# Kernel optimization log

Hardware: AMD Instinct MI355X
Metric: run time of the kernel (lower is better)

The kernel has to match this reference:

```python
import jax, jax.numpy as jnp
import numpy as np

N_HEADS = 32
N_KV = 8
N_REP = N_HEADS // N_KV  # 4
HEAD_DIM = 128
DIM = 4096


def _rope(x, cos, sin, start_pos):
    # x: (B, H, T, hd); cos/sin: (max_seq, hd//2)
    T = x.shape[2]
    c = jax.lax.dynamic_slice_in_dim(cos, start_pos, T, axis=0)[None, None]  # (1,1,T,hd/2)
    s = jax.lax.dynamic_slice_in_dim(sin, start_pos, T, axis=0)[None, None]
    x1, x2 = x[..., : HEAD_DIM // 2], x[..., HEAD_DIM // 2:]
    return jnp.concatenate([x1 * c - x2 * s, x2 * c + x1 * s], axis=-1)


def setup_inputs() -> dict:
    key = jax.random.key(0)
    ks = jax.random.split(key, 7)
    B, T = 1, 2048
    sc = 0.02
    return {
        "x": jax.random.normal(ks[0], (B, T, DIM), jnp.float32),
        "cos": jax.random.normal(ks[1], (T, HEAD_DIM // 2), jnp.float32),
        "sin": jax.random.normal(ks[2], (T, HEAD_DIM // 2), jnp.float32),
        "wq": jax.random.normal(ks[3], (N_HEADS * HEAD_DIM, DIM), jnp.float32) * sc,
        "wk": jax.random.normal(ks[4], (N_KV * HEAD_DIM, DIM), jnp.float32) * sc,
        "wv": jax.random.normal(ks[5], (N_KV * HEAD_DIM, DIM), jnp.float32) * sc,
        "wo": jax.random.normal(ks[6], (DIM, DIM), jnp.float32) * sc,
        "start_pos": 0,
    }


def reference(x, cos, sin, wq, wk, wv, wo, start_pos):
    B, T, _ = x.shape
    # Projections (nn.Linear: y = x @ W^T)
    q = (x @ wq.T).reshape(B, T, N_HEADS, HEAD_DIM).transpose(0, 2, 1, 3)  # (B,Hq,T,hd)
    k = (x @ wk.T).reshape(B, T, N_KV, HEAD_DIM).transpose(0, 2, 1, 3)    # (B,Hk,T,hd)
    v = (x @ wv.T).reshape(B, T, N_KV, HEAD_DIM).transpose(0, 2, 1, 3)
    q = _rope(q, cos, sin, start_pos)
    k = _rope(k, cos, sin, start_pos)
    # GQA: group query heads per kv head instead of materializing repeat_kv
    qg = q.reshape(B, N_KV, N_REP, T, HEAD_DIM)
    scale = 1.0 / jnp.sqrt(jnp.float32(HEAD_DIM))
    scores = jnp.einsum('bgrqd,bgkd->bgrqk', qg, k) * scale  # (B,Hk,rep,T,T)
    causal = jnp.tril(jnp.ones((T, T), dtype=bool))
    scores = jnp.where(causal, scores, jnp.finfo(scores.dtype).min)
    attn = jax.nn.softmax(scores, axis=-1)
    yg = jnp.einsum('bgrqk,bgkd->bgrqd', attn, v)  # (B,Hk,rep,T,hd)
    y = yg.reshape(B, N_HEADS, T, HEAD_DIM).transpose(0, 2, 1, 3).reshape(B, T, DIM)
    return y @ wo.T
```

## Files before the change

kernel.cpp:

```cpp
#include <hip/hip_runtime.h>
#include <hip/hip_bf16.h>
#include <stdint.h>

using bf16 = __hip_bfloat16;
using bf16x8 = __attribute__((ext_vector_type(8))) short;
using f32x4  = __attribute__((ext_vector_type(4))) float;

#define AS1 __attribute__((address_space(1)))
#define AS3 __attribute__((address_space(3)))

__device__ __forceinline__ void async_ld16(const void* g, void* l) {
    __builtin_amdgcn_global_load_lds((const AS1 void*)g, (AS3 void*)l, 16, 0, 0);
}

__device__ __forceinline__ f32x4 mfma_bf16(bf16x8 a, bf16x8 b, f32x4 c) {
    return __builtin_amdgcn_mfma_f32_16x16x32_bf16(a, b, c, 0, 0, 0);
}

__device__ __forceinline__ float sexp(float x) {
    return __expf(fmaxf(x, -80.0f));
}

template<int N> __device__ __forceinline__ float dpp_max16(float x) {
    int xi = __builtin_bit_cast(int, x);
    int yi = __builtin_amdgcn_update_dpp(xi, xi, 0x110 | N, 0xf, 0xf, false);
    return fmaxf(x, __builtin_bit_cast(float, yi));
}
template<int N> __device__ __forceinline__ float dpp_add16(float x) {
    int xi = __builtin_bit_cast(int, x);
    int yi = __builtin_amdgcn_update_dpp(0, xi, 0x110 | N, 0xf, 0xf, true);
    return x + __builtin_bit_cast(float, yi);
}
__device__ __forceinline__ float bcast15(float x) {
    return __builtin_bit_cast(float,
        __builtin_amdgcn_ds_swizzle(__builtin_bit_cast(int, x), 0x01F0));
}
__device__ __forceinline__ float redmax16(float x) {
    x = dpp_max16<1>(x); x = dpp_max16<2>(x);
    x = dpp_max16<4>(x); x = dpp_max16<8>(x);
    return bcast15(x);
}
__device__ __forceinline__ float redsum16(float x) {
    x = dpp_add16<1>(x); x = dpp_add16<2>(x);
    x = dpp_add16<4>(x); x = dpp_add16<8>(x);
    return bcast15(x);
}

__device__ __forceinline__ void cvt8(const float* p, bf16* d) {
    float4 lo = *(const float4*)p;
    float4 hi = *(const float4*)(p + 4);
    bf16 t8[8] = {__float2bfloat16(lo.x), __float2bfloat16(lo.y),
                  __float2bfloat16(lo.z), __float2bfloat16(lo.w),
                  __float2bfloat16(hi.x), __float2bfloat16(hi.y),
                  __float2bfloat16(hi.z), __float2bfloat16(hi.w)};
    *(bf16x8*)d = *(const bf16x8*)t8;
}

__global__ __launch_bounds__(256) void cvt4_k(const float* __restrict__ x,  bf16* __restrict__ xb,
                                              const float* __restrict__ wq, bf16* __restrict__ wqb,
                                              const float* __restrict__ wk, bf16* __restrict__ wkb,
                                              const float* __restrict__ wv, bf16* __restrict__ wvb) {
    int stride = gridDim.x * blockDim.x;
    for (int u = blockIdx.x * blockDim.x + threadIdx.x; u < 4194304; u += stride) {
        const float* s; bf16* d; size_t off;
        if (u < 1048576)      { s = x;  d = xb;  off = (size_t)u * 8; }
        else if (u < 3145728) { s = wq; d = wqb; off = (size_t)(u - 1048576) * 8; }
        else if (u < 3670016) { s = wk; d = wkb; off = (size_t)(u - 3145728) * 8; }
        else                  { s = wv; d = wvb; off = (size_t)(u - 3670016) * 8; }
        cvt8(s + off, d + off);
    }
}

__global__ __launch_bounds__(256) void cvt_f32_bf16(const float* __restrict__ src,
                                                    bf16* __restrict__ dst, int n8) {
    int stride = gridDim.x * blockDim.x;
    for (int u = blockIdx.x * blockDim.x + threadIdx.x; u < n8; u += stride)
        cvt8(src + (size_t)u * 8, dst + (size_t)u * 8);
}

template<bool SRCF32>
__device__ __forceinline__ void stage_tile(const void* __restrict__ src,
                                           bf16* __restrict__ s,
                                           int row0, int K, int k0, int tid) {
    if constexpr (SRCF32) {
        const float* g = (const float*)src;
        #pragma unroll
        for (int i = 0; i < 2; ++i) {
            int u = tid + 256 * i;
            int row = u >> 2, c8 = (u & 3) * 8;
            cvt8(g + (size_t)(row0 + row) * K + k0 + c8, &s[row * 32 + c8]);
        }
    } else {
        const bf16* g = (const bf16*)src;
        const int wave = tid >> 6, lane = tid & 63;
        const int c0 = wave * 64 + lane;
        const int r0 = c0 >> 2, cb0 = (c0 & 3) * 16;
        const int c1 = 256 + c0;
        const int r1 = c1 >> 2, cb1 = (c1 & 3) * 16;
        async_ld16((const char*)(g + (size_t)(row0 + r0) * K + k0) + cb0,
                   (char*)s + wave * 1024);
        async_ld16((const char*)(g + (size_t)(row0 + r1) * K + k0) + cb1,
                   (char*)s + 4096 + wave * 1024);
    }
}

template<bool AF32, bool BF32, int MODE>
__global__ __launch_bounds__(256) void gemm_bt(const void* __restrict__ A,
                                               const void* __restrict__ B,
                                               void* __restrict__ C,
                                               bf16* __restrict__ Qp,
                                               bf16* __restrict__ Kp,
                                               bf16* __restrict__ Vp,
                                               int M, int N, int K) {
    __shared__ bf16 sA[128 * 32];
    __shared__ bf16 sB[128 * 32];
    const int tid  = threadIdx.x;
    const int lane = tid & 63;
    const int wave = tid >> 6;
    const int m0 = blockIdx.y * 128;
    const int n0 = blockIdx.x * 128;
    const int mrow = (wave >> 1) * 64;
    const int ncol = (wave & 1) * 64;

    f32x4 acc[4][4] = {};

    for (int k0 = 0; k0 < K; k0 += 32) {
        __syncthreads();
        stage_tile<AF32>(A, sA, m0, K, k0, tid);
        stage_tile<BF32>(B, sB, n0, K, k0, tid);
        __syncthreads();

        bf16x8 af[4], bfr[4];
        #pragma unroll
        for (int i = 0; i < 4; ++i)
            af[i] = *(const bf16x8*)&sA[(mrow + i * 16 + (lane & 15)) * 32 + (lane >> 4) * 8];
        #pragma unroll
        for (int j = 0; j < 4; ++j)
            bfr[j] = *(const bf16x8*)&sB[(ncol + j * 16 + (lane & 15)) * 32 + (lane >> 4) * 8];
        #pragma unroll
        for (int i = 0; i < 4; ++i)
            #pragma unroll
            for (int j = 0; j < 4; ++j)
                acc[i][j] = mfma_bf16(af[i], bfr[j], acc[i][j]);
    }

    #pragma unroll
    for (int i = 0; i < 4; ++i)
        #pragma unroll
        for (int j = 0; j < 4; ++j)
            #pragma unroll
            for (int r = 0; r < 4; ++r) {
                int row = m0 + mrow + i * 16 + (lane >> 4) * 4 + r;
                int col = n0 + ncol + j * 16 + (lane & 15);
                float fv = acc[i][j][r];
                if constexpr (MODE == 0) {
                    ((bf16*)C)[(size_t)row * N + col] = __float2bfloat16(fv);
                } else if constexpr (MODE == 1) {
                    ((bf16*)C)[(size_t)col * M + row] = __float2bfloat16(fv);
                } else if constexpr (MODE == 2) {
                    bf16 v = __float2bfloat16(fv);
                    if (col < 4096)      Qp[(size_t)row * 4096 + col] = v;
                    else if (col < 5120) Kp[(size_t)row * 1024 + (col - 4096)] = v;
                    else                 Vp[(size_t)(col - 5120) * 2048 + row] = v;
                } else {
                    ((float*)C)[(size_t)row * N + col] = fv;
                }
            }
}

#define VMW(N) asm volatile("s_waitcnt vmcnt(" #N ")" ::: "memory")

#define PH(SA, SB, MH, NH, STG, WT) do {                                          \
    bf16x8 aF[2][2], bF[2][2];                                                    \
    _Pragma("unroll") for (int i2 = 0; i2 < 2; ++i2)                              \
      _Pragma("unroll") for (int kh = 0; kh < 2; ++kh)                            \
        aF[i2][kh] = *(const bf16x8*)((SA) + offA[(MH)*2 + i2][kh]);              \
    _Pragma("unroll") for (int j2 = 0; j2 < 2; ++j2)                              \
      _Pragma("unroll") for (int kh = 0; kh < 2; ++kh)                            \
        bF[j2][kh] = *(const bf16x8*)((SB) + offB[(NH)*2 + j2][kh]);              \
    STG;                                                                          \
    __builtin_amdgcn_s_barrier();                                                 \
    asm volatile("s_waitcnt lgkmcnt(0)" ::: "memory");                            \
    __builtin_amdgcn_sched_barrier(0);                                            \
    __builtin_amdgcn_s_setprio(1);                                                \
    _Pragma("unroll") for (int i2 = 0; i2 < 2; ++i2)                              \
      _Pragma("unroll") for (int j2 = 0; j2 < 2; ++j2)                            \
        _Pragma("unroll") for (int kh = 0; kh < 2; ++kh)                          \
          acc[(MH)*2 + i2][(NH)*2 + j2] =                                         \
              mfma_bf16(aF[i2][kh], bF[j2][kh], acc[(MH)*2 + i2][(NH)*2 + j2]);   \
    __builtin_amdgcn_s_setprio(0);                                                \
    __builtin_amdgcn_sched_barrier(0);                                            \
    WT;                                                                           \
    __builtin_amdgcn_s_barrier();                                                 \
  } while (0)

#define TILE(SA, SB, SA2, SB2, T2, DOST, WT) do {                                 \
    PH(SA, SB, 0, 0, if (DOST) stgA01(SA2, T2), );                                \
    PH(SA, SB, 0, 1, if (DOST) stgA23(SA2, T2), );                                \
    PH(SA, SB, 1, 0, if (DOST) stgB0(SB2, T2), );                                 \
    PH(SA, SB, 1, 1, if (DOST) stgB1(SB2, T2), WT);                               \
  } while (0)

template<int MODE>
__global__ __launch_bounds__(512, 1) void gemm_8p(const bf16* __restrict__ A,
                                                  const bf16* __restrict__ B,
                                                  void* __restrict__ C,
                                                  bf16* __restrict__ Qp,
                                                  bf16* __restrict__ Kp,
                                                  bf16* __restrict__ Vp,
                                                  int M, int N, int K) {
    __shared__ __align__(16) bf16 sA0[16384], sA1[16384], sA2[16384];
    __shared__ __align__(16) bf16 sB0[8192],  sB1[8192],  sB2[8192];

    const int tid  = threadIdx.x;
    const int lane = tid & 63;
    const int wave = tid >> 6;
    const int wr   = wave >> 1;
    const int wc   = wave & 1;
    const int m0 = blockIdx.y * 256;
    const int n0 = blockIdx.x * 128;
    const int NT = K >> 6;

    int offA[4][2], offB[4][2];
    {
        const int l15 = lane & 15, l4 = lane >> 4;
        #pragma unroll
        for (int i = 0; i < 4; ++i) {
            const int ra = wr * 64 + i * 16 + l15;
            const int rb = wc * 64 + i * 16 + l15;
            #pragma unroll
            for (int kh = 0; kh < 2; ++kh) {
                offA[i][kh] = ra * 64 + (((kh * 4 + l4) ^ (ra & 7)) * 8);
                offB[i][kh] = rb * 64 + (((kh * 4 + l4) ^ (rb & 7)) * 8);
            }
        }
    }

    const int rloc = tid >> 3;
    const int qsw  = (tid & 7) ^ (rloc & 7);
    const bf16* gA0 = A + (size_t)(m0 +   0 + rloc) * K + qsw * 8;
    const bf16* gA1 = A + (size_t)(m0 +  64 + rloc) * K + qsw * 8;
    const bf16* gA2 = A + (size_t)(m0 + 128 + rloc) * K + qsw * 8;
    const bf16* gA3 = A + (size_t)(m0 + 192 + rloc) * K + qsw * 8;
    const bf16* gB0 = B + (size_t)(n0 +   0 + rloc) * K + qsw * 8;
    const bf16* gB1 = B + (size_t)(n0 +  64 + rloc) * K + qsw * 8;
    const int w512 = wave * 512;

    auto stgA01 = [&](bf16* dst, int kt) __attribute__((always_inline)) {
        async_ld16(gA0 + kt * 64, dst + w512);
        async_ld16(gA1 + kt * 64, dst + 4096 + w512);
    };
    auto stgA23 = [&](bf16* dst, int kt) __attribute__((always_inline)) {
        async_ld16(gA2 + kt * 64, dst + 8192 + w512);
        async_ld16(gA3 + kt * 64, dst + 12288 + w512);
    };
    auto stgB0 = [&](bf16* dst, int kt) __attribute__((always_inline)) {
        async_ld16(gB0 + kt * 64, dst + w512);
    };
    auto stgB1 = [&](bf16* dst, int kt) __attribute__((always_inline)) {
        async_ld16(gB1 + kt * 64, dst + 4096 + w512);
    };

    f32x4 acc[4][4] = {};

    stgA01(sA0, 0); stgA23(sA0, 0); stgB0(sB0, 0); stgB1(sB0, 0);
    stgA01(sA1, 1); stgA23(sA1, 1); stgB0(sB1, 1); stgB1(sB1, 1);
    VMW(6);
    __builtin_amdgcn_s_barrier();
    asm volatile("" ::: "memory");
    __builtin_amdgcn_sched_barrier(0);

    int t = 0;
    for (; t < NT - 6; t += 3) {
        TILE(sA0, sB0, sA2, sB2, t + 2, true, VMW(6));
        TILE(sA1, sB1, sA0, sB0, t + 3, true, VMW(6));
        TILE(sA2, sB2, sA1, sB1, t + 4, true, VMW(6));
    }
    TILE(sA0, sB0, sA2, sB2, NT - 2, true,  VMW(6));
    TILE(sA1, sB1, sA0, sB0, NT - 1, true,  VMW(6));
    TILE(sA2, sB2, sA0, sB0, 0,      false, VMW(0));
    TILE(sA0, sB0, sA1, sB1, 0,      false, );
    asm volatile("s_waitcnt vmcnt(0)" ::: "memory");

    #pragma unroll
    for (int i = 0; i < 4; ++i)
        #pragma unroll
        for (int j = 0; j < 4; ++j)
            #pragma unroll
            for (int r = 0; r < 4; ++r) {
                int row = m0 + wr * 64 + i * 16 + (lane >> 4) * 4 + r;
                int col = n0 + wc * 64 + j * 16 + (lane & 15);
                float fv = acc[i][j][r];
                if constexpr (MODE == 2) {
                    bf16 v = __float2bfloat16(fv);
                    if (col < 4096)      Qp[(size_t)row * 4096 + col] = v;
                    else if (col < 5120) Kp[(size_t)row * 1024 + (col - 4096)] = v;
                    else                 Vp[(size_t)(col - 5120) * 2048 + row] = v;
                } else {
                    ((float*)C)[(size_t)row * N + col] = fv;
                }
            }
}

__global__ __launch_bounds__(256) void rope_all(bf16* __restrict__ Q,
                                                bf16* __restrict__ K,
                                                const float* __restrict__ cosp,
                                                const float* __restrict__ sinp,
                                                const int* __restrict__ spp) {
    int idx = blockIdx.x * blockDim.x + threadIdx.x;
    int d = idx & 63;
    int h = (idx >> 6) % 40;
    int t = idx / (64 * 40);
    int sp = *spp;
    float c = cosp[(size_t)(t + sp) * 64 + d];
    float s = sinp[(size_t)(t + sp) * 64 + d];
    bf16* row = (h < 32) ? (Q + (size_t)t * 4096 + h * 128)
                         : (K + (size_t)t * 1024 + (h - 32) * 128);
    float x1 = __bfloat162float(row[d]);
    float x2 = __bfloat162float(row[64 + d]);
    row[d]      = __float2bfloat16(x1 * c - x2 * s);
    row[64 + d] = __float2bfloat16(x2 * c + x1 * s);
}

#define NEG_SENT (-1.0e9f)
__global__ __launch_bounds__(256) void attn_k(const bf16* __restrict__ Q,
                                              const bf16* __restrict__ K,
                                              const bf16* __restrict__ VT,
                                              bf16* __restrict__ Y) {
    constexpr int SKS = 136;
    constexpr int SVS = 72;
    __shared__ bf16 sK[64 * SKS];
    __shared__ bf16 sVT[128 * SVS];

    const int tid  = threadIdx.x;
    const int lane = tid & 63;
    const int wave = tid >> 6;
    const int qtile = 31 - (blockIdx.x >> 5);
    const int head  = blockIdx.x & 31;
    const int g     = head >> 2;
    const int qrow0 = qtile * 64 + wave * 16;
    bf16* sPw = sK + wave * 1152;

    bf16x8 qf[4];
    {
        const bf16* qbase = Q + (size_t)(qrow0 + (lane & 15)) * 4096 + head * 128;
        #pragma unroll
        for (int kk = 0; kk < 4; ++kk)
            qf[kk] = *(const bf16x8*)(qbase + kk * 32 + (lane >> 4) * 8);
    }

    float m_i[4], l_i[4];
    #pragma unroll
    for (int r = 0; r < 4; ++r) { m_i[r] = NEG_SENT; l_i[r] = 0.f; }
    f32x4 o[8] = {};
    const float scale = 0.08838834764831845f;

    for (int kt = 0; kt <= qtile; ++kt) {
        const int kt0 = kt * 64;
        __syncthreads();
        #pragma unroll
        for (int i = 0; i < 4; ++i) {
            int c = i * 256 + tid;
            {
                int row = c >> 4, ch = c & 15;
                *(uint4*)&sK[row * SKS + ch * 8] =
                    *(const uint4*)(K + (size_t)(kt0 + row) * 1024 + g * 128 + ch * 8);
            }
            {
                int row = c >> 3, ch = c & 7;
                *(uint4*)&sVT[row * SVS + ch * 8] =
                    *(const uint4*)(VT + (size_t)(g * 128 + row) * 2048 + kt0 + ch * 8);
            }
        }
        __syncthreads();

        f32x4 s[4];
        #pragma unroll
        for (int j = 0; j < 4; ++j) {
            f32x4 a = {};
            #pragma unroll
            for (int kk = 0; kk < 4; ++kk) {
                bf16x8 kfrag = *(const bf16x8*)&sK[(j * 16 + (lane & 15)) * SKS +
                                                   kk * 32 + (lane >> 4) * 8];
                a = mfma_bf16(qf[kk], kfrag, a);
            }
            s[j] = a;
        }

        #pragma unroll
        for (int j = 0; j < 4; ++j) {
            int tk = kt0 + j * 16 + (lane & 15);
            #pragma unroll
            for (int r = 0; r < 4; ++r) {
                int tq = qrow0 + (lane >> 4) * 4 + r;
                float v = s[j][r] * scale;
                s[j][r] = (tk > tq) ? NEG_SENT : v;
            }
        }

        #pragma unroll
        for (int r = 0; r < 4; ++r) {
            float mx = fmaxf(fmaxf(s[0][r], s[1][r]), fmaxf(s[2][r], s[3][r]));
            mx = redmax16(mx);
            float mn = fmaxf(m_i[r], mx);
            float alpha = sexp(m_i[r] - mn);
            m_i[r] = mn;
            float rs = 0.f;
            #pragma unroll
            for (int j = 0; j < 4; ++j) {
                float pv = sexp(s[j][r] - mn);
                s[j][r] = pv;
                rs += pv;
            }
            l_i[r] = l_i[r] * alpha + rs;
            #pragma unroll
            for (int j2 = 0; j2 < 8; ++j2) o[j2][r] *= alpha;
        }

        __syncthreads();

        #pragma unroll
        for (int j = 0; j < 4; ++j)
            #pragma unroll
            for (int r = 0; r < 4; ++r)
                sPw[((lane >> 4) * 4 + r) * SVS + j * 16 + (lane & 15)] =
                    __float2bfloat16(s[j][r]);
        __asm__ volatile("s_waitcnt lgkmcnt(0)" ::: "memory");

        #pragma unroll
        for (int kk2 = 0; kk2 < 2; ++kk2) {
            bf16x8 pf = *(const bf16x8*)&sPw[(lane & 15) * SVS + kk2 * 32 + (lane >> 4) * 8];
            #pragma unroll
            for (int j2 = 0; j2 < 8; ++j2) {
                bf16x8 vf = *(const bf16x8*)&sVT[(j2 * 16 + (lane & 15)) * SVS +
                                                 kk2 * 32 + (lane >> 4) * 8];
                o[j2] = mfma_bf16(pf, vf, o[j2]);
            }
        }
    }

    #pragma unroll
    for (int r = 0; r < 4; ++r) l_i[r] = redsum16(l_i[r]);
    #pragma unroll
    for (int j2 = 0; j2 < 8; ++j2)
        #pragma unroll
        for (int r = 0; r < 4; ++r) {
            int t   = qrow0 + (lane >> 4) * 4 + r;
            int col = head * 128 + j2 * 16 + (lane & 15);
            Y[(size_t)t * 4096 + col] = __float2bfloat16(o[j2][r] / l_i[r]);
        }
}

extern "C" void kernel_launch(void* const* d_in, const int* in_sizes, int n_in,
                              void* d_out, int out_size, void* d_ws, size_t ws_size,
                              hipStream_t stream) {
    const float* x    = (const float*)d_in[0];
    const float* cosp = (const float*)d_in[1];
    const float* sinp = (const float*)d_in[2];
    const float* wq   = (const float*)d_in[3];
    const float* wk   = (const float*)d_in[4];
    const float* wv   = (const float*)d_in[5];
    const float* wo   = (const float*)d_in[6];
    const int*   sp   = (const int*)d_in[7];
    float* out = (float*)d_out;

    char* ws = (char*)d_ws;
    bf16* Qb = (bf16*)d_out;

    const size_t NEED = 92274688;
    if (ws_size >= NEED) {
        bf16* xb   = (bf16*)(ws);
        bf16* wqkv = (bf16*)(ws + (16u << 20));
        bf16* wob  = wqkv;
        bf16* Kb   = (bf16*)(ws + (64u << 20));
        bf16* VT   = (bf16*)(ws + (68u << 20));
        bf16* Yb   = (bf16*)(ws + (72u << 20));

        cvt4_k<<<dim3(4096), 256, 0, stream>>>(x, xb, wq, wqkv,
                                               wk, wqkv + 16777216, wv, wqkv + 20971520);

        gemm_8p<2><<<dim3(48, 8), 512, 0, stream>>>(
            xb, wqkv, nullptr, Qb, Kb, VT, 2048, 6144, 4096);

        cvt_f32_bf16<<<dim3(4096), 256, 0, stream>>>(wo, wob, 2097152);

        rope_all<<<dim3(2048 * 40 * 64 / 256), 256, 0, stream>>>(Qb, Kb, cosp, sinp, sp);

        attn_k<<<dim3(1024), 256, 0, stream>>>(Qb, Kb, VT, Yb);

        gemm_8p<3><<<dim3(32, 8), 512, 0, stream>>>(
            Yb, wob, out, nullptr, nullptr, nullptr, 2048, 4096, 4096);
    } else {
        bf16* Kb = (bf16*)(ws);
        bf16* VT = (bf16*)(ws + (4u << 20));
        bf16* Yb = (bf16*)(ws + (8u << 20));

        gemm_bt<true, true, 0><<<dim3(32, 16), 256, 0, stream>>>(
            x, wq, Qb, nullptr, nullptr, nullptr, 2048, 4096, 4096);
        gemm_bt<true, true, 0><<<dim3(8, 16), 256, 0, stream>>>(
            x, wk, Kb, nullptr, nullptr, nullptr, 2048, 1024, 4096);
        gemm_bt<true, true, 1><<<dim3(8, 16), 256, 0, stream>>>(
            x, wv, VT, nullptr, nullptr, nullptr, 2048, 1024, 4096);

        rope_all<<<dim3(2048 * 40 * 64 / 256), 256, 0, stream>>>(Qb, Kb, cosp, sinp, sp);

        attn_k<<<dim3(1024), 256, 0, stream>>>(Qb, Kb, VT, Yb);

        gemm_bt<false, true, 3><<<dim3(32, 16), 256, 0, stream>>>(
            Yb, wo, out, nullptr, nullptr, nullptr, 2048, 4096, 4096);
    }
}
```

Before: 568.6 us.

## Restructure GEMM tile loop into two K-half phases with one barrier

Replaces the four per-quadrant phases, each with two barriers, by one tile step. It loads all A/B fragments for both K halves, issues all four async global->LDS stages together, and runs the first half of the MFMAs after a partial lgkmcnt wait. The goal is fewer workgroup barriers per tile and overlap of the second half's LDS reads with the first half's MFMAs. It uses more fragment registers, and issuing all stages at once changes the vmcnt accounting that the VMW(6) waits rely on.

```diff
diff --git a/kernel.cpp b/kernel.cpp
--- a/kernel.cpp
+++ b/kernel.cpp
@@ -169,36 +169,39 @@
 }
 
 #define VMW(N) asm volatile("s_waitcnt vmcnt(" #N ")" ::: "memory")
-
-#define PH(SA, SB, MH, NH, STG, WT) do {                                          \
-    bf16x8 aF[2][2], bF[2][2];                                                    \
-    _Pragma("unroll") for (int i2 = 0; i2 < 2; ++i2)                              \
-      _Pragma("unroll") for (int kh = 0; kh < 2; ++kh)                            \
-        aF[i2][kh] = *(const bf16x8*)((SA) + offA[(MH)*2 + i2][kh]);              \
-    _Pragma("unroll") for (int j2 = 0; j2 < 2; ++j2)                              \
-      _Pragma("unroll") for (int kh = 0; kh < 2; ++kh)                            \
-        bF[j2][kh] = *(const bf16x8*)((SB) + offB[(NH)*2 + j2][kh]);              \
-    STG;                                                                          \
-    __builtin_amdgcn_s_barrier();                                                 \
+#define SCB    __builtin_amdgcn_sched_barrier(0)
+
+#define TILE2(SA, SB, SA2, SB2, T2, DOST, WT) do {                                \
+    bf16x8 aF0[4], bF0[4], aF1[4], bF1[4];                                        \
+    _Pragma("unroll") for (int i = 0; i < 4; ++i)                                 \
+        aF0[i] = *(const bf16x8*)((SA) + offA[i][0]);                             \
+    _Pragma("unroll") for (int j = 0; j < 4; ++j)                                 \
+        bF0[j] = *(const bf16x8*)((SB) + offB[j][0]);                             \
+    SCB;                                                                          \
+    _Pragma("unroll") for (int i = 0; i < 4; ++i)                                 \
+        aF1[i] = *(const bf16x8*)((SA) + offA[i][1]);                             \
+    _Pragma("unroll") for (int j = 0; j < 4; ++j)                                 \
+        bF1[j] = *(const bf16x8*)((SB) + offB[j][1]);                             \
+    SCB;                                                                          \
+    if (DOST) { stgA01(SA2, T2); stgA23(SA2, T2); stgB0(SB2, T2); stgB1(SB2, T2); } \
+    asm volatile("s_waitcnt lgkmcnt(8)" ::: "memory");                            \
+    SCB;                                                                          \
+    __builtin_amdgcn_s_setprio(1);                                                \
+    _Pragma("unroll") for (int i = 0; i < 4; ++i)                                 \
+      _Pragma("unroll") for (int j = 0; j < 4; ++j)                               \
+        acc[i][j] = mfma_bf16(aF0[i], bF0[j], acc[i][j]);                         \
+    __builtin_amdgcn_s_setprio(0);                                                \
+    SCB;                                                                          \
     asm volatile("s_waitcnt lgkmcnt(0)" ::: "memory");                            \
-    __builtin_amdgcn_sched_barrier(0);                                            \
+    SCB;                                                                          \
     __builtin_amdgcn_s_setprio(1);                                                \
-    _Pragma("unroll") for (int i2 = 0; i2 < 2; ++i2)                              \
-      _Pragma("unroll") for (int j2 = 0; j2 < 2; ++j2)                            \
-        _Pragma("unroll") for (int kh = 0; kh < 2; ++kh)                          \
-          acc[(MH)*2 + i2][(NH)*2 + j2] =                                         \
-              mfma_bf16(aF[i2][kh], bF[j2][kh], acc[(MH)*2 + i2][(NH)*2 + j2]);   \
+    _Pragma("unroll") for (int i = 0; i < 4; ++i)                                 \
+      _Pragma("unroll") for (int j = 0; j < 4; ++j)                               \
+        acc[i][j] = mfma_bf16(aF1[i], bF1[j], acc[i][j]);                         \
     __builtin_amdgcn_s_setprio(0);                                                \
-    __builtin_amdgcn_sched_barrier(0);                                            \
+    SCB;                                                                          \
     WT;                                                                           \
     __builtin_amdgcn_s_barrier();                                                 \
-  } while (0)
-
-#define TILE(SA, SB, SA2, SB2, T2, DOST, WT) do {                                 \
-    PH(SA, SB, 0, 0, if (DOST) stgA01(SA2, T2), );                                \
-    PH(SA, SB, 0, 1, if (DOST) stgA23(SA2, T2), );                                \
-    PH(SA, SB, 1, 0, if (DOST) stgB0(SB2, T2), );                                 \
-    PH(SA, SB, 1, 1, if (DOST) stgB1(SB2, T2), WT);                               \
   } while (0)
 
 template<int MODE>
@@ -268,18 +271,18 @@
     VMW(6);
     __builtin_amdgcn_s_barrier();
     asm volatile("" ::: "memory");
-    __builtin_amdgcn_sched_barrier(0);
+    SCB;
 
     int t = 0;
     for (; t < NT - 6; t += 3) {
-        TILE(sA0, sB0, sA2, sB2, t + 2, true, VMW(6));
-        TILE(sA1, sB1, sA0, sB0, t + 3, true, VMW(6));
-        TILE(sA2, sB2, sA1, sB1, t + 4, true, VMW(6));
-    }
-    TILE(sA0, sB0, sA2, sB2, NT - 2, true,  VMW(6));
-    TILE(sA1, sB1, sA0, sB0, NT - 1, true,  VMW(6));
-    TILE(sA2, sB2, sA0, sB0, 0,      false, VMW(0));
-    TILE(sA0, sB0, sA1, sB1, 0,      false, );
+        TILE2(sA0, sB0, sA2, sB2, t + 2, true, VMW(6));
+        TILE2(sA1, sB1, sA0, sB0, t + 3, true, VMW(6));
+        TILE2(sA2, sB2, sA1, sB1, t + 4, true, VMW(6));
+    }
+    TILE2(sA0, sB0, sA2, sB2, NT - 2, true,  VMW(6));
+    TILE2(sA1, sB1, sA0, sB0, NT - 1, true,  VMW(6));
+    TILE2(sA2, sB2, sA0, sB0, 0,      false, VMW(0));
+    TILE2(sA0, sB0, sA1, sB1, 0,      false, );
     asm volatile("s_waitcnt vmcnt(0)" ::: "memory");
 
     #pragma unroll
```

Result: faster. 480.9 us (-15.4%).
